# Performance work log

Measured on AMD Instinct MI355X. Metric: run time of the kernel, lower is better.

The kernel has to match this reference:

```python
import jax, jax.numpy as jnp
import numpy as np

LEVEL_SHAPES = [(100, 134), (50, 67), (25, 34), (13, 17)]  # (H, W) per feature level
NH, NL, NP, D, DFF = 8, 4, 4, 256, 1024
DH = D // NH
LTOT = sum(h * w for h, w in LEVEL_SHAPES)  # 17821
BS, NQ = 4, 300


def _ln(x, w, b):
    m = x.mean(-1, keepdims=True)
    v = ((x - m) ** 2).mean(-1, keepdims=True)
    return (x - m) / jnp.sqrt(v + 1e-5) * w + b


def _mha(q, k, v, in_w, in_b, out_w, out_b):
    B, N, _ = q.shape
    wq, wk, wv = jnp.split(in_w, 3, axis=0)
    bq, bk, bv = jnp.split(in_b, 3)
    qh = (q @ wq.T + bq).reshape(B, N, NH, DH)
    kh = (k @ wk.T + bk).reshape(B, N, NH, DH)
    vh = (v @ wv.T + bv).reshape(B, N, NH, DH)
    a = jax.nn.softmax(jnp.einsum('bqhd,bkhd->bhqk', qh, kh) / float(np.sqrt(DH)), axis=-1)
    o = jnp.einsum('bhqk,bkhd->bqhd', a, vh).reshape(B, N, D)
    return o @ out_w.T + out_b


def _bilinear(img, grid):
    # img [B,C,H,W]; grid [B,N,2] in [-1,1]; align_corners=False, zero padding
    B, C, H, W = img.shape
    x = (grid[..., 0] + 1.0) * 0.5 * W - 0.5
    y = (grid[..., 1] + 1.0) * 0.5 * H - 0.5
    x0f = jnp.floor(x); y0f = jnp.floor(y)
    wx = x - x0f; wy = y - y0f
    x0 = x0f.astype(jnp.int32); y0 = y0f.astype(jnp.int32)
    flat = img.reshape(B, C, H * W)

    def gather(xi, yi):
        m = ((xi >= 0) & (xi < W) & (yi >= 0) & (yi < H)).astype(img.dtype)
        idx = jnp.clip(yi, 0, H - 1) * W + jnp.clip(xi, 0, W - 1)
        g = jnp.take_along_axis(flat, jnp.broadcast_to(idx[:, None, :], (B, C, idx.shape[-1])), axis=2)
        return g * m[:, None, :]

    return (gather(x0, y0) * ((1 - wx) * (1 - wy))[:, None]
            + gather(x0 + 1, y0) * (wx * (1 - wy))[:, None]
            + gather(x0, y0 + 1) * ((1 - wx) * wy)[:, None]
            + gather(x0 + 1, y0 + 1) * (wx * wy)[:, None])


def _msdeform(value, loc, aw):
    # value [B,L,NH,DH]; loc [B,Nq,NH,NL,NP,2] in [0,1]; aw [B,Nq,NH,NL,NP]
    B, Nq = loc.shape[0], loc.shape[1]
    outs = []
    start = 0
    for l, (Hl, Wl) in enumerate(LEVEL_SHAPES):
        v = value[:, start:start + Hl * Wl].transpose(0, 2, 3, 1).reshape(B * NH, DH, Hl, Wl)
        g = (2.0 * loc[:, :, :, l] - 1.0).transpose(0, 2, 1, 3, 4).reshape(B * NH, Nq * NP, 2)
        outs.append(_bilinear(v, g).reshape(B * NH, DH, Nq, NP))
        start += Hl * Wl
    samp = jnp.stack(outs, axis=3)  # [B*NH, DH, Nq, NL, NP]
    w = aw.transpose(0, 2, 1, 3, 4).reshape(B * NH, 1, Nq, NL, NP)
    out = (samp * w).sum(axis=(3, 4))  # [B*NH, DH, Nq]
    return out.reshape(B, NH, DH, Nq).transpose(0, 3, 1, 2).reshape(B, Nq, D)


def _deform_branch(q, ref, src_other, vw, vb, ow, ob, aww, awb, outw, outb):
    B, Nq, _ = q.shape
    value = (src_other @ vw.T + vb).reshape(B, -1, NH, DH)
    off = (q @ ow.T + ob).reshape(B, Nq, NH, NL, NP, 2)
    aw = jax.nn.softmax((q @ aww.T + awb).reshape(B, Nq, NH, NL * NP), axis=-1).reshape(B, Nq, NH, NL, NP)
    norm = jnp.array([[w, h] for h, w in LEVEL_SHAPES], dtype=q.dtype)  # (W,H) per level
    loc = ref[:, :, None, :, None, :] + off / norm[None, None, None, :, None, :]
    return _msdeform(value, loc, aw) @ outw.T + outb


def reference(tgt_RGB, tgt_T, query_pos_RGB, query_pos_T, ref_RGB, ref_T, src_RGB, src_T,
              sa_in_w, sa_in_b, sa_out_w, sa_out_b, ln_w, ln_b,
              ffn_w1, ffn_b1, ffn_w2, ffn_b2,
              val_w, val_b, off_w, off_b, aw_w, aw_b, cout_w, cout_b):
    # --- dual self-attention (eval mode: dropout = identity) ---
    q_RGB = tgt_RGB + query_pos_RGB
    q_T = tgt_T + query_pos_T
    sa_RGB = _mha(q_RGB, q_RGB, tgt_RGB, sa_in_w[0], sa_in_b[0], sa_out_w[0], sa_out_b[0])
    sa_T = _mha(q_T, q_T, tgt_T, sa_in_w[1], sa_in_b[1], sa_out_w[1], sa_out_b[1])
    tgt_RGB = _ln(tgt_RGB + sa_RGB, ln_w[0, 1], ln_b[0, 1])  # norm2_RGB
    tgt_T = _ln(tgt_T + sa_T, ln_w[1, 1], ln_b[1, 1])        # norm2_T
    # --- interactive multi-scale deformable cross-attn: RGB queries sample T memory & vice versa ---
    qc_RGB = tgt_RGB + query_pos_RGB
    qc_T = tgt_T + query_pos_T
    t2_RGB = _deform_branch(qc_RGB, ref_RGB, src_T, val_w[0], val_b[0], off_w[0], off_b[0], aw_w[0], aw_b[0], cout_w[0], cout_b[0])
    t2_T = _deform_branch(qc_T, ref_T, src_RGB, val_w[1], val_b[1], off_w[1], off_b[1], aw_w[1], aw_b[1], cout_w[1], cout_b[1])
    F_RGB, F_T = t2_RGB, t2_T
    # cross residuals exactly as in the torch layer (note the modality swap)
    r = tgt_T + t2_RGB
    t = r + t2_T
    tgt_RGB = _ln(r, ln_w[0, 0], ln_b[0, 0])  # norm1_RGB
    tgt_T = _ln(t, ln_w[1, 0], ln_b[1, 0])    # norm1_T
    # --- FFNs ---
    tgt_RGB = _ln(tgt_RGB + (jax.nn.relu(tgt_RGB @ ffn_w1[0].T + ffn_b1[0]) @ ffn_w2[0].T + ffn_b2[0]), ln_w[0, 2], ln_b[0, 2])
    tgt_T = _ln(tgt_T + (jax.nn.relu(tgt_T @ ffn_w1[1].T + ffn_b1[1]) @ ffn_w2[1].T + ffn_b2[1]), ln_w[1, 2], ln_b[1, 2])
    return tgt_RGB, tgt_T, F_RGB, F_T


def setup_inputs() -> dict:
    key = jax.random.key(0)
    ks = jax.random.split(key, 24)
    s = 0.05
    w = lambda k, shp: jax.random.normal(k, shp, dtype=jnp.float32) * s
    return {
        'tgt_RGB': jax.random.normal(ks[0], (BS, NQ, D), jnp.float32),
        'tgt_T': jax.random.normal(ks[1], (BS, NQ, D), jnp.float32),
        'query_pos_RGB': jax.random.normal(ks[2], (BS, NQ, D), jnp.float32),
        'query_pos_T': jax.random.normal(ks[3], (BS, NQ, D), jnp.float32),
        'ref_RGB': jax.random.uniform(ks[4], (BS, NQ, NL, 2), jnp.float32),
        'ref_T': jax.random.uniform(ks[5], (BS, NQ, NL, 2), jnp.float32),
        'src_RGB': jax.random.normal(ks[6], (BS, LTOT, D), jnp.float32),
        'src_T': jax.random.normal(ks[7], (BS, LTOT, D), jnp.float32),
        'sa_in_w': w(ks[8], (2, 3 * D, D)),
        'sa_in_b': jnp.zeros((2, 3 * D), jnp.float32),
        'sa_out_w': w(ks[9], (2, D, D)),
        'sa_out_b': jnp.zeros((2, D), jnp.float32),
        'ln_w': jnp.ones((2, 3, D), jnp.float32),
        'ln_b': jnp.zeros((2, 3, D), jnp.float32),
        'ffn_w1': w(ks[10], (2, DFF, D)),
        'ffn_b1': jnp.zeros((2, DFF), jnp.float32),
        'ffn_w2': w(ks[11], (2, D, DFF)),
        'ffn_b2': jnp.zeros((2, D), jnp.float32),
        'val_w': w(ks[12], (2, D, D)),
        'val_b': jnp.zeros((2, D), jnp.float32),
        'off_w': w(ks[13], (2, NH * NL * NP * 2, D)),
        'off_b': jax.random.normal(ks[14], (2, NH * NL * NP * 2), jnp.float32) * 0.5,
        'aw_w': w(ks[15], (2, NH * NL * NP, D)),
        'aw_b': jnp.zeros((2, NH * NL * NP), jnp.float32),
        'cout_w': w(ks[16], (2, D, D)),
        'cout_b': jnp.zeros((2, D), jnp.float32),
    }
```

## Files before the change

kernel.cpp:

```cpp
#include <hip/hip_runtime.h>
#include <hip/hip_bf16.h>
#include <cstddef>
#include <math.h>

#define NTOK 1200
#define LTOT_C 17821
#define MVAL 71284
#define STOK (NTOK * 256)

typedef __attribute__((ext_vector_type(8))) short bhalf8;
typedef __attribute__((ext_vector_type(4))) float f32x4;

static __device__ __forceinline__ short f2bf(float f) {
    unsigned u = __builtin_bit_cast(unsigned, f);
    u += 0x7fffu + ((u >> 16) & 1u);
    return (short)(u >> 16);
}
static __device__ __forceinline__ float bf2f(short s) {
    unsigned u = ((unsigned)(unsigned short)s) << 16;
    return __builtin_bit_cast(float, u);
}
static __device__ __forceinline__ bhalf8 cvt8(float4 a, float4 b) {
    bhalf8 h;
    h[0] = f2bf(a.x); h[1] = f2bf(a.y); h[2] = f2bf(a.z); h[3] = f2bf(a.w);
    h[4] = f2bf(b.x); h[5] = f2bf(b.y); h[6] = f2bf(b.z); h[7] = f2bf(b.w);
    return h;
}
static __device__ __forceinline__ void gload_lds16(const void* g, void* l) {
    __builtin_amdgcn_global_load_lds(
        (const __attribute__((address_space(1))) void*)g,
        (__attribute__((address_space(3))) void*)l, 16, 0, 0);
}

struct PrepArgs {
    const float* s[10]; short* d[10]; int n[10];
    const float* tgt0; const float* tgt1; const float* pos0; const float* pos1;
    short* qb_bf; short* tgtb;
    const float* off_b; const float* aw_b; float* baw;
};
__global__ __launch_bounds__(256) void prep_all(PrepArgs a) {
    const int task = blockIdx.y;
    if (task < 10) {
        const float* s = a.s[task];
        short* d = a.d[task];
        const int n = a.n[task];
        for (int base = (blockIdx.x * 256 + threadIdx.x) * 8; base < n;
             base += gridDim.x * 256 * 8) {
            const float4 f0 = *reinterpret_cast<const float4*>(s + base);
            const float4 f1 = *reinterpret_cast<const float4*>(s + base + 4);
            *reinterpret_cast<bhalf8*>(d + base) = cvt8(f0, f1);
        }
        return;
    }
    const int z = task - 10;
    if (blockIdx.x == 0 && z == 0) {
        for (int i = threadIdx.x; i < 768; i += 256) {
            const int zz = i / 384, j = i - zz * 384;
            a.baw[i] = (j < 256) ? a.off_b[zz * 256 + j] : a.aw_b[zz * 128 + (j - 256)];
        }
    }
    const float* tg = z ? a.tgt1 : a.tgt0;
    const float* ps = z ? a.pos1 : a.pos0;
    const int base = (blockIdx.x * 256 + threadIdx.x) * 8;
    if (base >= STOK) return;
    const float4 t0 = *reinterpret_cast<const float4*>(tg + base);
    const float4 t1 = *reinterpret_cast<const float4*>(tg + base + 4);
    const float4 p0 = *reinterpret_cast<const float4*>(ps + base);
    const float4 p1 = *reinterpret_cast<const float4*>(ps + base + 4);
    float4 s0 = make_float4(t0.x + p0.x, t0.y + p0.y, t0.z + p0.z, t0.w + p0.w);
    float4 s1 = make_float4(t1.x + p1.x, t1.y + p1.y, t1.z + p1.z, t1.w + p1.w);
    *reinterpret_cast<bhalf8*>(a.qb_bf + (size_t)z * STOK + base) = cvt8(s0, s1);
    *reinterpret_cast<bhalf8*>(a.tgtb + (size_t)z * STOK + base) = cvt8(t0, t1);
}

__global__ __launch_bounds__(256) void val_inproj(
    const float* __restrict__ A0, const float* __restrict__ A1,
    const short* __restrict__ val_bf, const float* __restrict__ val_b,
    short* __restrict__ valb,
    const short* __restrict__ qb_bf, const short* __restrict__ tgtb,
    const short* __restrict__ sa_in_bf, const float* __restrict__ sa_in_b,
    float* __restrict__ qkv)
{
    __shared__ alignas(16) short As[64 * 64];
    __shared__ alignas(16) short Bs[2][128 * 64];
    const int t = threadIdx.x;
    const int wave = t >> 6, lane = t & 63;
    const int l15 = lane & 15, l4 = lane >> 4;
    const int wr = wave >> 1, wc = wave & 1;
    const int nr8 = lane >> 3, q8 = lane & 7;
    const int bi = blockIdx.x;

    if (bi >= 228) {
        const int i = bi - 228;
        const int widx = (i & 7) * 557 + (i >> 3);
        const int x = widx & 1;
        const int yz = widx >> 1;
        const int z = yz / 1114;
        const int y = yz - z * 1114;
        const float* A = z ? A1 : A0;
        const short* W = val_bf + (size_t)z * 65536;
        const float* bz = val_b + z * 256;
        short* Cz = valb + (size_t)z * MVAL * 256;
        const int bm = y * 64, bn = x * 128;
        f32x4 acc[2][4] = {};

        auto stageW = [&](int k0, int buf) {
            #pragma unroll
            for (int ii = 0; ii < 4; ++ii) {
                const int c = wave * 4 + ii;
                const int n = c * 8 + nr8;
                gload_lds16(W + (size_t)(bn + n) * 256 + k0 + ((q8 ^ nr8) << 3),
                            (char*)&Bs[buf][0] + c * 1024);
            }
        };
        float4 paf[2][2];
        auto issueA = [&](int k0) {
            #pragma unroll
            for (int ii = 0; ii < 2; ++ii) {
                const int G = t + ii * 256;
                const int m = G >> 3, g = G & 7;
                const int row = min(bm + m, MVAL - 1);
                const float* s = A + (size_t)row * 256 + k0 + g * 8;
                paf[ii][0] = *reinterpret_cast<const float4*>(s);
                paf[ii][1] = *reinterpret_cast<const float4*>(s + 4);
            }
        };
        auto commitA = [&]() {
            #pragma unroll
            for (int ii = 0; ii < 2; ++ii) {
                const int G = t + ii * 256;
                const int m = G >> 3, g = G & 7;
                *reinterpret_cast<bhalf8*>(&As[m * 64 + ((g ^ (m & 7)) << 3)]) =
                    cvt8(paf[ii][0], paf[ii][1]);
            }
        };
        auto compute = [&](int wbuf) {
            #pragma unroll
            for (int kf = 0; kf < 2; ++kf) {
                bhalf8 af[2], bfv[4];
                #pragma unroll
                for (int mf = 0; mf < 2; ++mf) {
                    const int m = wr * 32 + (mf << 4) + l15;
                    const int g = ((kf << 2) + l4) ^ (m & 7);
                    af[mf] = *reinterpret_cast<const bhalf8*>(&As[m * 64 + (g << 3)]);
                }
                #pragma unroll
                for (int nf = 0; nf < 4; ++nf) {
                    const int n = (wc << 6) + (nf << 4) + l15;
                    const int g = ((kf << 2) + l4) ^ (n & 7);
                    bfv[nf] = *reinterpret_cast<const bhalf8*>(&Bs[wbuf][n * 64 + (g << 3)]);
                }
                #pragma unroll
                for (int mf = 0; mf < 2; ++mf)
                    #pragma unroll
                    for (int nf = 0; nf < 4; ++nf)
                        acc[mf][nf] = __builtin_amdgcn_mfma_f32_16x16x32_bf16(
                            af[mf], bfv[nf], acc[mf][nf], 0, 0, 0);
            }
        };

        issueA(0);
        stageW(0, 0);
        commitA();
        __syncthreads();
        #pragma unroll
        for (int ks = 0; ks < 4; ++ks) {
            const int cur = ks & 1, nxt = cur ^ 1;
            if (ks + 1 < 4) {
                issueA((ks + 1) << 6);
                stageW((ks + 1) << 6, nxt);
            }
            compute(cur);
            if (ks + 1 < 4) {
                __syncthreads();
                commitA();
                __syncthreads();
            }
        }

        float br[4];
        #pragma unroll
        for (int nf = 0; nf < 4; ++nf) br[nf] = bz[bn + (wc << 6) + (nf << 4) + l15];
        #pragma unroll
        for (int mf = 0; mf < 2; ++mf) {
            #pragma unroll
            for (int j = 0; j < 4; ++j) {
                const int row = bm + wr * 32 + (mf << 4) + (l4 << 2) + j;
                if (row >= MVAL) continue;
                const int colbase = bn + (wc << 6);
                #pragma unroll
                for (int nf = 0; nf < 4; ++nf)
                    Cz[(size_t)row * 256 + colbase + (nf << 4) + l15] =
                        f2bf(acc[mf][nf][j] + br[nf]);
            }
        }
    } else {
        const int z = bi / 114;
        const int r = bi - z * 114;
        const int x = r / 19;
        const int y = r - x * 19;
        const short* Abase = ((x < 4) ? qb_bf : tgtb) + (size_t)z * STOK;
        const short* W = sa_in_bf + (size_t)z * 196608;
        const float* bz = sa_in_b + z * 768;
        const int bm = y * 64, bn = x * 128;
        f32x4 acc[2][4] = {};

        auto stageW = [&](int k0, int buf) {
            #pragma unroll
            for (int ii = 0; ii < 4; ++ii) {
                const int c = wave * 4 + ii;
                const int n = c * 8 + nr8;
                gload_lds16(W + (size_t)(bn + n) * 256 + k0 + ((q8 ^ nr8) << 3),
                            (char*)&Bs[buf][0] + c * 1024);
            }
        };
        bhalf8 pab[2];
        auto issueA = [&](int k0) {
            #pragma unroll
            for (int ii = 0; ii < 2; ++ii) {
                const int G = t + ii * 256;
                const int m = G >> 3, g = G & 7;
                const int row = min(bm + m, NTOK - 1);
                pab[ii] = *reinterpret_cast<const bhalf8*>(
                    Abase + (size_t)row * 256 + k0 + g * 8);
            }
        };
        auto commitA = [&]() {
            #pragma unroll
            for (int ii = 0; ii < 2; ++ii) {
                const int G = t + ii * 256;
                const int m = G >> 3, g = G & 7;
                *reinterpret_cast<bhalf8*>(&As[m * 64 + ((g ^ (m & 7)) << 3)]) = pab[ii];
            }
        };
        auto compute = [&](int wbuf) {
            #pragma unroll
            for (int kf = 0; kf < 2; ++kf) {
                bhalf8 af[2], bfv[4];
                #pragma unroll
                for (int mf = 0; mf < 2; ++mf) {
                    const int m = wr * 32 + (mf << 4) + l15;
                    const int g = ((kf << 2) + l4) ^ (m & 7);
                    af[mf] = *reinterpret_cast<const bhalf8*>(&As[m * 64 + (g << 3)]);
                }
                #pragma unroll
                for (int nf = 0; nf < 4; ++nf) {
                    const int n = (wc << 6) + (nf << 4) + l15;
                    const int g = ((kf << 2) + l4) ^ (n & 7);
                    bfv[nf] = *reinterpret_cast<const bhalf8*>(&Bs[wbuf][n * 64 + (g << 3)]);
                }
                #pragma unroll
                for (int mf = 0; mf < 2; ++mf)
                    #pragma unroll
                    for (int nf = 0; nf < 4; ++nf)
                        acc[mf][nf] = __builtin_amdgcn_mfma_f32_16x16x32_bf16(
                            af[mf], bfv[nf], acc[mf][nf], 0, 0, 0);
            }
        };

        issueA(0);
        stageW(0, 0);
        commitA();
        __syncthreads();
        #pragma unroll
        for (int ks = 0; ks < 4; ++ks) {
            const int cur = ks & 1, nxt = cur ^ 1;
            if (ks + 1 < 4) {
                issueA((ks + 1) << 6);
                stageW((ks + 1) << 6, nxt);
            }
            compute(cur);
            if (ks + 1 < 4) {
                __syncthreads();
                commitA();
                __syncthreads();
            }
        }

        float* Cz = qkv + (size_t)z * 921600;
        float br[4];
        #pragma unroll
        for (int nf = 0; nf < 4; ++nf) br[nf] = bz[bn + (wc << 6) + (nf << 4) + l15];
        #pragma unroll
        for (int mf = 0; mf < 2; ++mf) {
            #pragma unroll
            for (int j = 0; j < 4; ++j) {
                const int row = bm + wr * 32 + (mf << 4) + (l4 << 2) + j;
                if (row >= NTOK) continue;
                const int colbase = bn + (wc << 6);
                #pragma unroll
                for (int nf = 0; nf < 4; ++nf)
                    Cz[(size_t)row * 768 + colbase + (nf << 4) + l15] = acc[mf][nf][j] + br[nf];
            }
        }
    }
}

template<bool HASRES, bool RELU, bool OUT_BF16, int BM, int NK>
__global__ __launch_bounds__(256) void gemm_bf16(
    const short* __restrict__ Av, size_t aStrideZ, int lda,
    const short* __restrict__ Wv, size_t wStrideZ, int ldw,
    const float* __restrict__ bias, size_t biasStrideZ,
    const float* __restrict__ Res0, const float* __restrict__ Res1, int ldr,
    void* __restrict__ Cv, size_t cStrideZ, int ldc,
    int M)
{
    constexpr int MFR = BM / 32;
    constexpr int ACW = BM / 32;
    __shared__ alignas(16) short As[2][BM * 64];
    __shared__ alignas(16) short Bs[2][128 * 64];
    const int z = blockIdx.z;
    const short* W = Wv + (size_t)z * wStrideZ;
    const float* bz = bias + (size_t)z * biasStrideZ;
    const int t = threadIdx.x;
    const int wave = t >> 6, lane = t & 63;
    const int l15 = lane & 15, l4 = lane >> 4;
    const int wr = wave >> 1, wc = wave & 1;
    const int bm = blockIdx.y * BM, bn = blockIdx.x * 128;
    f32x4 acc[MFR][4] = {};

    const int nr8 = lane >> 3, q8 = lane & 7;
    auto stageW = [&](int k0, int buf) {
        #pragma unroll
        for (int i = 0; i < 4; ++i) {
            const int c = wave * 4 + i;
            const int n = c * 8 + nr8;
            gload_lds16(W + (size_t)(bn + n) * ldw + k0 + ((q8 ^ nr8) << 3),
                        (char*)&Bs[buf][0] + c * 1024);
        }
    };
    auto stageA = [&](int k0, int buf) {
        #pragma unroll
        for (int i = 0; i < ACW; ++i) {
            const int c = wave * ACW + i;
            const int m = c * 8 + nr8;
            const int row = min(bm + m, M - 1);
            gload_lds16(Av + (size_t)z * aStrideZ + (size_t)row * lda + k0 + ((q8 ^ (m & 7)) << 3),
                        (char*)&As[buf][0] + c * 1024);
        }
    };
    auto compute = [&](int buf) {
        #pragma unroll
        for (int kf = 0; kf < 2; ++kf) {
            bhalf8 af[MFR], bfv[4];
            #pragma unroll
            for (int mf = 0; mf < MFR; ++mf) {
                const int m = wr * (BM / 2) + (mf << 4) + l15;
                const int g = ((kf << 2) + l4) ^ (m & 7);
                af[mf] = *reinterpret_cast<const bhalf8*>(&As[buf][m * 64 + (g << 3)]);
            }
            #pragma unroll
            for (int nf = 0; nf < 4; ++nf) {
                const int n = (wc << 6) + (nf << 4) + l15;
                const int g = ((kf << 2) + l4) ^ (n & 7);
                bfv[nf] = *reinterpret_cast<const bhalf8*>(&Bs[buf][n * 64 + (g << 3)]);
            }
            #pragma unroll
            for (int mf = 0; mf < MFR; ++mf)
                #pragma unroll
                for (int nf = 0; nf < 4; ++nf)
                    acc[mf][nf] = __builtin_amdgcn_mfma_f32_16x16x32_bf16(
                        af[mf], bfv[nf], acc[mf][nf], 0, 0, 0);
        }
    };

    stageA(0, 0);
    stageW(0, 0);
    __syncthreads();
    #pragma unroll
    for (int ks = 0; ks < NK; ++ks) {
        const int cur = ks & 1, nxt = cur ^ 1;
        if (ks + 1 < NK) {
            stageA((ks + 1) << 6, nxt);
            stageW((ks + 1) << 6, nxt);
        }
        compute(cur);
        __syncthreads();
    }

    const float* Rz = HASRES ? (z ? Res1 : Res0) : nullptr;
    float br[4];
    #pragma unroll
    for (int nf = 0; nf < 4; ++nf) br[nf] = bz[bn + (wc << 6) + (nf << 4) + l15];
    #pragma unroll
    for (int mf = 0; mf < MFR; ++mf) {
        #pragma unroll
        for (int j = 0; j < 4; ++j) {
            const int row = bm + wr * (BM / 2) + (mf << 4) + (l4 << 2) + j;
            if (row >= M) continue;
            const int colbase = bn + (wc << 6);
            #pragma unroll
            for (int nf = 0; nf < 4; ++nf) {
                const int col = colbase + (nf << 4) + l15;
                float v = acc[mf][nf][j] + br[nf];
                if (HASRES) v += Rz[(size_t)row * ldr + col];
                if (RELU) v = fmaxf(v, 0.f);
                if (OUT_BF16)
                    ((short*)Cv + (size_t)z * cStrideZ)[(size_t)row * ldc + col] = f2bf(v);
                else
                    ((float*)Cv + (size_t)z * cStrideZ)[(size_t)row * ldc + col] = v;
            }
        }
    }
}

__global__ __launch_bounds__(256) void attn2_kernel(
    const float* __restrict__ qkv_base, short* __restrict__ out_base)
{
    const float scale = 0.17677669529663687f;
    const float* qkv = qkv_base + (size_t)blockIdx.z * 921600;
    short* outp = out_base + (size_t)blockIdx.z * STOK;
    const int b = blockIdx.y >> 3, h = blockIdx.y & 7;
    const int t = threadIdx.x;
    const int ql = t & 31;
    const int kg = t >> 5;
    const int q = blockIdx.x * 32 + ql;
    const bool act = q < 300;
    const float* base = qkv + (size_t)b * 300 * 768;

    float qreg[32];
    if (act) {
        const float4* qp = reinterpret_cast<const float4*>(base + (size_t)q * 768 + h * 32);
        #pragma unroll
        for (int d4 = 0; d4 < 8; ++d4) {
            const float4 v = qp[d4];
            qreg[d4 * 4 + 0] = v.x; qreg[d4 * 4 + 1] = v.y;
            qreg[d4 * 4 + 2] = v.z; qreg[d4 * 4 + 3] = v.w;
        }
    }
    __shared__ float Ks[64][32];
    __shared__ float Vs[64][32];
    float m = -1e30f, l = 0.f, o[32];
    #pragma unroll
    for (int d = 0; d < 32; ++d) o[d] = 0.f;

    for (int k0 = 0; k0 < 300; k0 += 64) {
        const int cnt = min(64, 300 - k0);
        __syncthreads();
        for (int i = t; i < cnt * 32; i += 256) {
            const int kr = i >> 5, d = i & 31;
            Ks[kr][d] = base[(size_t)(k0 + kr) * 768 + 256 + h * 32 + d];
            Vs[kr][d] = base[(size_t)(k0 + kr) * 768 + 512 + h * 32 + d];
        }
        __syncthreads();
        if (act) {
            for (int kk = kg; kk < cnt; kk += 8) {
                const float4* krow = reinterpret_cast<const float4*>(&Ks[kk][0]);
                float s = 0.f;
                #pragma unroll
                for (int d4 = 0; d4 < 8; ++d4) {
                    const float4 kv = krow[d4];
                    s += qreg[d4 * 4 + 0] * kv.x + qreg[d4 * 4 + 1] * kv.y
                       + qreg[d4 * 4 + 2] * kv.z + qreg[d4 * 4 + 3] * kv.w;
                }
                s *= scale;
                const float4* vrow = reinterpret_cast<const float4*>(&Vs[kk][0]);
                if (s <= m) {
                    const float e = __expf(s - m);
                    l += e;
                    #pragma unroll
                    for (int d4 = 0; d4 < 8; ++d4) {
                        const float4 vv = vrow[d4];
                        o[d4 * 4 + 0] += e * vv.x; o[d4 * 4 + 1] += e * vv.y;
                        o[d4 * 4 + 2] += e * vv.z; o[d4 * 4 + 3] += e * vv.w;
                    }
                } else {
                    const float c = __expf(m - s);
                    l = l * c + 1.f;
                    #pragma unroll
                    for (int d4 = 0; d4 < 8; ++d4) {
                        const float4 vv = vrow[d4];
                        o[d4 * 4 + 0] = o[d4 * 4 + 0] * c + vv.x;
                        o[d4 * 4 + 1] = o[d4 * 4 + 1] * c + vv.y;
                        o[d4 * 4 + 2] = o[d4 * 4 + 2] * c + vv.z;
                        o[d4 * 4 + 3] = o[d4 * 4 + 3] * c + vv.w;
                    }
                    m = s;
                }
            }
        }
    }
    __shared__ float pm[32][8];
    __shared__ float pl[32][8];
    __shared__ float po[8][32][33];
    pm[ql][kg] = m; pl[ql][kg] = l;
    #pragma unroll
    for (int d = 0; d < 32; ++d) po[kg][d][ql] = o[d];
    __syncthreads();
    if (kg == 0) {
        float M = pm[ql][0];
        #pragma unroll
        for (int i = 1; i < 8; ++i) M = fmaxf(M, pm[ql][i]);
        float L = 0.f;
        #pragma unroll
        for (int i = 0; i < 8; ++i) L += pl[ql][i] * __expf(pm[ql][i] - M);
        const float invL = 1.f / L;
        #pragma unroll
        for (int i = 0; i < 8; ++i) pm[ql][i] = __expf(pm[ql][i] - M) * invL;
    }
    __syncthreads();
    if (act) {
        #pragma unroll
        for (int dd = 0; dd < 4; ++dd) {
            const int d = kg * 4 + dd;
            float v = 0.f;
            #pragma unroll
            for (int i = 0; i < 8; ++i) v += pm[ql][i] * po[i][d][ql];
            outp[((size_t)b * 300 + q) * 256 + h * 32 + d] = f2bf(v);
        }
    }
}

#define LN_BODY(vexpr, widx)                                                  \
    const int row = blockIdx.x, t = threadIdx.x, z = blockIdx.y;              \
    (void)z;                                                                  \
    const int i = row * 256 + t;                                              \
    const float v = (vexpr);                                                  \
    __shared__ float r1[4], r2[4];                                            \
    float s = v;                                                              \
    _Pragma("unroll")                                                         \
    for (int o = 32; o; o >>= 1) s += __shfl_xor(s, o);                       \
    if ((t & 63) == 0) r1[t >> 6] = s;                                        \
    __syncthreads();                                                          \
    const float mean = (r1[0] + r1[1] + r1[2] + r1[3]) * (1.f / 256.f);       \
    const float dd = v - mean;                                                \
    float sq = dd * dd;                                                       \
    _Pragma("unroll")                                                         \
    for (int o = 32; o; o >>= 1) sq += __shfl_xor(sq, o);                     \
    if ((t & 63) == 0) r2[t >> 6] = sq;                                       \
    __syncthreads();                                                          \
    const float var = (r2[0] + r2[1] + r2[2] + r2[3]) * (1.f / 256.f);        \
    const float y = dd * rsqrtf(var + 1e-5f) * ln_w[(widx) * 256 + t]         \
                    + ln_b[(widx) * 256 + t];

__global__ __launch_bounds__(256) void ln2_fused(
    const float* __restrict__ presum, const float* __restrict__ pos0,
    const float* __restrict__ pos1, const float* __restrict__ ln_w,
    const float* __restrict__ ln_b, short* __restrict__ qc_bf,
    float* __restrict__ tgt2T)
{
    LN_BODY(presum[(size_t)z * STOK + i], z * 3 + 1)
    const float* pos = z ? pos1 : pos0;
    qc_bf[(size_t)z * STOK + i] = f2bf(y + pos[i]);
    if (z == 1) tgt2T[i] = y;
}

__global__ __launch_bounds__(256) void ln1_fused(
    const float* __restrict__ tgt2T, const float* __restrict__ out2,
    const float* __restrict__ out3, const float* __restrict__ ln_w,
    const float* __restrict__ ln_b, short* __restrict__ ln1b,
    float* __restrict__ ln1f)
{
    LN_BODY(tgt2T[row * 256 + t] + out2[row * 256 + t] + (z ? out3[row * 256 + t] : 0.f), z * 3 + 0)
    ln1b[(size_t)z * STOK + i] = f2bf(y);
    ln1f[(size_t)z * STOK + i] = y;
}

__global__ __launch_bounds__(256) void ln3_kernel(
    const float* __restrict__ ffny, const float* __restrict__ ln_w,
    const float* __restrict__ ln_b, float* __restrict__ o0,
    float* __restrict__ o1)
{
    LN_BODY(ffny[(size_t)z * STOK + i], z * 3 + 2)
    (z ? o1 : o0)[i] = y;
}

__global__ __launch_bounds__(256) void sample_kernel(
    const short* __restrict__ valb, const float* __restrict__ oaw,
    const float* __restrict__ ref0, const float* __restrict__ ref1,
    short* __restrict__ out)
{
    const int HL[4] = {100, 50, 25, 13};
    const int WL[4] = {134, 67, 34, 17};
    const int ST[4] = {0, 13400, 16750, 17600};
    const int z = blockIdx.y;
    const int t = threadIdx.x;
    const int wave = t >> 6, lane = t & 63;
    const int qi = wave >> 1, hh = wave & 1;
    const int pg = lane >> 4;
    const int h4 = (lane >> 2) & 3;
    const int dl2 = lane & 3;
    const int h = hh * 4 + h4;
    const int bq = blockIdx.x * 2 + qi;
    const int b = bq / 300;
    const float* op = oaw + ((size_t)z * NTOK + bq) * 384;
    const float* offp = op + h * 32;
    const float* awp  = op + 256 + h * 16;
    const float* refp = (z ? ref1 : ref0) + (size_t)bq * 8;
    const short* vb = valb + (size_t)z * MVAL * 256 + (size_t)b * LTOT_C * 256;
    const int co = h * 32 + dl2 * 8;

    float w16[16];
    float mx = -1e30f;
    #pragma unroll
    for (int i = 0; i < 16; ++i) { w16[i] = awp[i]; mx = fmaxf(mx, w16[i]); }
    float ssum = 0.f;
    #pragma unroll
    for (int i = 0; i < 16; ++i) { w16[i] = __expf(w16[i] - mx); ssum += w16[i]; }
    const float sinv = 1.f / ssum;

    float a[8] = {};
    auto tap = [&](bool cond, int ridx, float wv) {
        if (cond) {
            const bhalf8 sv = *reinterpret_cast<const bhalf8*>(vb + (size_t)ridx * 256 + co);
            #pragma unroll
            for (int dd = 0; dd < 8; ++dd) a[dd] += wv * bf2f(sv[dd]);
        }
    };
    #pragma unroll
    for (int l = 0; l < 4; ++l) {
        const int Wl = WL[l], Hl = HL[l];
        const float rx = refp[l * 2] * (float)Wl - 0.5f;
        const float ry = refp[l * 2 + 1] * (float)Hl - 0.5f;
        const float px = rx + offp[(l * 4 + pg) * 2];
        const float py = ry + offp[(l * 4 + pg) * 2 + 1];
        const float wgt = w16[l * 4 + pg] * sinv;
        const float x0f = floorf(px), y0f = floorf(py);
        const float wx = px - x0f, wy = py - y0f;
        const int x0 = (int)x0f, y0 = (int)y0f;
        const bool xa = (x0 >= 0) & (x0 < Wl);
        const bool xb = (x0 >= -1) & (x0 < Wl - 1);
        const bool ya = (y0 >= 0) & (y0 < Hl);
        const bool yb = (y0 >= -1) & (y0 < Hl - 1);
        const int rbase = ST[l] + y0 * Wl + x0;
        tap(ya & xa, rbase,          wgt * (1.f - wx) * (1.f - wy));
        tap(ya & xb, rbase + 1,      wgt * wx * (1.f - wy));
        tap(yb & xa, rbase + Wl,     wgt * (1.f - wx) * wy);
        tap(yb & xb, rbase + Wl + 1, wgt * wx * wy);
    }
    #pragma unroll
    for (int dd = 0; dd < 8; ++dd) {
        a[dd] += __shfl_xor(a[dd], 16);
        a[dd] += __shfl_xor(a[dd], 32);
    }
    if (pg == 0) {
        bhalf8 o8;
        #pragma unroll
        for (int dd = 0; dd < 8; ++dd) o8[dd] = f2bf(a[dd]);
        *reinterpret_cast<bhalf8*>(&out[((size_t)z * NTOK + bq) * 256 + co]) = o8;
    }
}

extern "C" void kernel_launch(void* const* d_in, const int* in_sizes, int n_in,
                              void* d_out, int out_size, void* d_ws, size_t ws_size,
                              hipStream_t stream) {
    const float* tgt[2] = {(const float*)d_in[0], (const float*)d_in[1]};
    const float* pos[2] = {(const float*)d_in[2], (const float*)d_in[3]};
    const float* ref[2] = {(const float*)d_in[4], (const float*)d_in[5]};
    const float* src[2] = {(const float*)d_in[6], (const float*)d_in[7]};
    const float* sa_in_w  = (const float*)d_in[8];
    const float* sa_in_b  = (const float*)d_in[9];
    const float* sa_out_w = (const float*)d_in[10];
    const float* sa_out_b = (const float*)d_in[11];
    const float* ln_w = (const float*)d_in[12];
    const float* ln_b = (const float*)d_in[13];
    const float* ffn_w1 = (const float*)d_in[14];
    const float* ffn_b1 = (const float*)d_in[15];
    const float* ffn_w2 = (const float*)d_in[16];
    const float* ffn_b2 = (const float*)d_in[17];
    const float* val_w = (const float*)d_in[18];
    const float* val_b = (const float*)d_in[19];
    const float* off_w = (const float*)d_in[20];
    const float* off_b = (const float*)d_in[21];
    const float* aw_w = (const float*)d_in[22];
    const float* aw_b = (const float*)d_in[23];
    const float* cout_w = (const float*)d_in[24];
    const float* cout_b = (const float*)d_in[25];

    char* base = (char*)d_ws;
    size_t off = 0;
    auto alloc = [&](size_t bytes) -> char* {
        char* p = base + off;
        off += (bytes + 255) & ~(size_t)255;
        return p;
    };
    short* wbf   = (short*)alloc((size_t)2031616 * 2);
    float* baw   = (float*)alloc(768 * 4);
    short* qb_bf = (short*)alloc((size_t)2 * STOK * 2);
    short* tgtb  = (short*)alloc((size_t)2 * STOK * 2);
    float* qkv   = (float*)alloc((size_t)2 * 921600 * 4);
    short* attno = (short*)alloc((size_t)2 * STOK * 2);
    float* presum= (float*)alloc((size_t)2 * STOK * 4);
    short* qc_bf = (short*)alloc((size_t)2 * STOK * 2);
    float* tgt2T = (float*)alloc((size_t)STOK * 4);
    float* oawb  = (float*)alloc((size_t)2 * NTOK * 384 * 4);
    short* valb  = (short*)alloc((size_t)2 * MVAL * 256 * 2);
    short* samp  = (short*)alloc((size_t)2 * STOK * 2);
    short* ln1b  = (short*)alloc((size_t)2 * STOK * 2);
    float* ln1f  = (float*)alloc((size_t)2 * STOK * 4);
    short* ffnh  = (short*)alloc((size_t)2 * NTOK * 1024 * 2);
    float* ffny  = (float*)alloc((size_t)2 * STOK * 4);

    short* sa_in_bf  = wbf + 0;
    short* sa_out_bf = wbf + 393216;
    short* ffn1_bf   = wbf + 524288;
    short* ffn2_bf   = wbf + 1048576;
    short* val_bf    = wbf + 1572864;
    short* cout_bf   = wbf + 1703936;
    short* oaw_bf    = wbf + 1835008;

    float* out0 = (float*)d_out;
    float* out1 = out0 + STOK;
    float* out2 = out1 + STOK;
    float* out3 = out2 + STOK;

    const dim3 b256(256);

    PrepArgs pa;
    pa.s[0] = sa_in_w;        pa.d[0] = sa_in_bf;       pa.n[0] = 393216;
    pa.s[1] = sa_out_w;       pa.d[1] = sa_out_bf;      pa.n[1] = 131072;
    pa.s[2] = ffn_w1;         pa.d[2] = ffn1_bf;        pa.n[2] = 524288;
    pa.s[3] = ffn_w2;         pa.d[3] = ffn2_bf;        pa.n[3] = 524288;
    pa.s[4] = val_w;          pa.d[4] = val_bf;         pa.n[4] = 131072;
    pa.s[5] = cout_w;         pa.d[5] = cout_bf;        pa.n[5] = 131072;
    pa.s[6] = off_w;          pa.d[6] = oaw_bf;         pa.n[6] = 65536;
    pa.s[7] = aw_w;           pa.d[7] = oaw_bf + 65536; pa.n[7] = 32768;
    pa.s[8] = off_w + 65536;  pa.d[8] = oaw_bf + 98304; pa.n[8] = 65536;
    pa.s[9] = aw_w + 32768;   pa.d[9] = oaw_bf + 163840;pa.n[9] = 32768;
    pa.tgt0 = tgt[0]; pa.tgt1 = tgt[1]; pa.pos0 = pos[0]; pa.pos1 = pos[1];
    pa.qb_bf = qb_bf; pa.tgtb = tgtb;
    pa.off_b = off_b; pa.aw_b = aw_b; pa.baw = baw;
    prep_all<<<dim3(150, 12), b256, 0, stream>>>(pa);

    val_inproj<<<dim3(4684), b256, 0, stream>>>(
        src[1], src[0], val_bf, val_b, valb,
        qb_bf, tgtb, sa_in_bf, sa_in_b, qkv);

    attn2_kernel<<<dim3(10, 32, 2), b256, 0, stream>>>(qkv, attno);

    gemm_bf16<true, false, false, 64, 4><<<dim3(2, 19, 2), b256, 0, stream>>>(
        attno, (size_t)STOK, 256, sa_out_bf, 65536, 256, sa_out_b, 256,
        tgt[0], tgt[1], 256, presum, (size_t)STOK, 256, NTOK);

    ln2_fused<<<dim3(NTOK, 2), b256, 0, stream>>>(presum, pos[0], pos[1], ln_w, ln_b, qc_bf, tgt2T);

    gemm_bf16<false, false, false, 64, 4><<<dim3(3, 19, 2), b256, 0, stream>>>(
        qc_bf, (size_t)STOK, 256, oaw_bf, 98304, 256, baw, 384,
        nullptr, nullptr, 0, oawb, (size_t)NTOK * 384, 384, NTOK);

    sample_kernel<<<dim3(600, 2), b256, 0, stream>>>(valb, oawb, ref[0], ref[1], samp);

    gemm_bf16<false, false, false, 64, 4><<<dim3(2, 19, 2), b256, 0, stream>>>(
        samp, (size_t)STOK, 256, cout_bf, 65536, 256, cout_b, 256,
        nullptr, nullptr, 0, out2, (size_t)STOK, 256, NTOK);

    ln1_fused<<<dim3(NTOK, 2), b256, 0, stream>>>(tgt2T, out2, out3, ln_w, ln_b, ln1b, ln1f);

    gemm_bf16<false, true, true, 64, 4><<<dim3(8, 19, 2), b256, 0, stream>>>(
        ln1b, (size_t)STOK, 256, ffn1_bf, 262144, 256, ffn_b1, 1024,
        nullptr, nullptr, 0, ffnh, (size_t)NTOK * 1024, 1024, NTOK);

    gemm_bf16<true, false, false, 64, 16><<<dim3(2, 19, 2), b256, 0, stream>>>(
        ffnh, (size_t)NTOK * 1024, 1024, ffn2_bf, 262144, 1024, ffn_b2, 256,
        ln1f, ln1f + STOK, 256, ffny, (size_t)STOK, 256, NTOK);

    ln3_kernel<<<dim3(NTOK, 2), b256, 0, stream>>>(ffny, ln_w, ln_b, out0, out1);
}
```

Measured before the change: 178.4 us.

## Fuse LayerNorm into full-row GEMM epilogues for out-proj and FFN2

Adds a gemm_ln kernel in which each block computes all 256 output columns for 64 rows, so the residual add and LayerNorm can be done in the epilogue with a cross-wave shared-memory reduction. It replaces the sa_out GEMM plus ln2_fused and the FFN2 GEMM plus ln3_kernel. This removes two launches and the fp32 intermediate round trips. In exchange the grid shrinks to 38 blocks (from 76), the W tile is loaded with no double buffering, and variance is computed as E[x^2]-mean^2.

```diff
diff --git a/kernel.cpp b/kernel.cpp
--- a/kernel.cpp
+++ b/kernel.cpp
@@ -399,6 +399,160 @@
                     ((short*)Cv + (size_t)z * cStrideZ)[(size_t)row * ldc + col] = f2bf(v);
                 else
                     ((float*)Cv + (size_t)z * cStrideZ)[(size_t)row * ldc + col] = v;
+            }
+        }
+    }
+}
+
+template<int NK, int MODE>
+__global__ __launch_bounds__(256) void gemm_ln(
+    const short* __restrict__ Av, size_t aStrideZ, int lda,
+    const short* __restrict__ Wv, size_t wStrideZ,
+    const float* __restrict__ bias,
+    const float* __restrict__ Res0, const float* __restrict__ Res1,
+    const float* __restrict__ ln_w, const float* __restrict__ ln_b,
+    const float* __restrict__ pos0, const float* __restrict__ pos1,
+    short* __restrict__ qc_bf, float* __restrict__ tgt2T,
+    float* __restrict__ out0, float* __restrict__ out1,
+    int M)
+{
+    __shared__ alignas(16) short As[64 * 64];
+    __shared__ alignas(16) short Bs[256 * 64];
+    __shared__ float red[2][4][64];
+    const int z = blockIdx.z;
+    const short* W = Wv + (size_t)z * wStrideZ;
+    const float* bz = bias + (size_t)z * 256;
+    const float* Rz = z ? Res1 : Res0;
+    const int li = z * 3 + (MODE == 0 ? 1 : 2);
+    const int t = threadIdx.x;
+    const int wave = t >> 6, lane = t & 63;
+    const int l15 = lane & 15, l4 = lane >> 4;
+    const int nr8 = lane >> 3, q8 = lane & 7;
+    const int bm = blockIdx.y * 64;
+    f32x4 acc[4][4] = {};
+
+    auto stageW = [&](int k0) {
+        #pragma unroll
+        for (int i = 0; i < 8; ++i) {
+            const int c = wave * 8 + i;
+            const int n = c * 8 + nr8;
+            gload_lds16(W + (size_t)n * lda + k0 + ((q8 ^ nr8) << 3),
+                        (char*)&Bs[0] + c * 1024);
+        }
+    };
+    bhalf8 pab[2];
+    auto issueA = [&](int k0) {
+        #pragma unroll
+        for (int ii = 0; ii < 2; ++ii) {
+            const int G = t + ii * 256;
+            const int m = G >> 3, g = G & 7;
+            const int row = min(bm + m, M - 1);
+            pab[ii] = *reinterpret_cast<const bhalf8*>(
+                Av + (size_t)z * aStrideZ + (size_t)row * lda + k0 + g * 8);
+        }
+    };
+    auto commitA = [&]() {
+        #pragma unroll
+        for (int ii = 0; ii < 2; ++ii) {
+            const int G = t + ii * 256;
+            const int m = G >> 3, g = G & 7;
+            *reinterpret_cast<bhalf8*>(&As[m * 64 + ((g ^ (m & 7)) << 3)]) = pab[ii];
+        }
+    };
+    auto compute = [&]() {
+        #pragma unroll
+        for (int kf = 0; kf < 2; ++kf) {
+            bhalf8 af[4], bfv[4];
+            #pragma unroll
+            for (int mf = 0; mf < 4; ++mf) {
+                const int m = (mf << 4) + l15;
+                const int g = ((kf << 2) + l4) ^ (m & 7);
+                af[mf] = *reinterpret_cast<const bhalf8*>(&As[m * 64 + (g << 3)]);
+            }
+            #pragma unroll
+            for (int nf = 0; nf < 4; ++nf) {
+                const int n = (wave << 6) + (nf << 4) + l15;
+                const int g = ((kf << 2) + l4) ^ (n & 7);
+                bfv[nf] = *reinterpret_cast<const bhalf8*>(&Bs[n * 64 + (g << 3)]);
+            }
+            #pragma unroll
+            for (int mf = 0; mf < 4; ++mf)
+                #pragma unroll
+                for (int nf = 0; nf < 4; ++nf)
+                    acc[mf][nf] = __builtin_amdgcn_mfma_f32_16x16x32_bf16(
+                        af[mf], bfv[nf], acc[mf][nf], 0, 0, 0);
+        }
+    };
+
+    for (int ks = 0; ks < NK; ++ks) {
+        issueA(ks << 6);
+        stageW(ks << 6);
+        commitA();
+        __syncthreads();
+        compute();
+        __syncthreads();
+    }
+
+    float br[4];
+    #pragma unroll
+    for (int nf = 0; nf < 4; ++nf) br[nf] = bz[(wave << 6) + (nf << 4) + l15];
+    #pragma unroll
+    for (int mf = 0; mf < 4; ++mf) {
+        #pragma unroll
+        for (int j = 0; j < 4; ++j) {
+            const int row = bm + (mf << 4) + (l4 << 2) + j;
+            const int rr = min(row, M - 1);
+            #pragma unroll
+            for (int nf = 0; nf < 4; ++nf) {
+                const int col = (wave << 6) + (nf << 4) + l15;
+                acc[mf][nf][j] += br[nf] + Rz[(size_t)rr * 256 + col];
+            }
+        }
+    }
+    #pragma unroll
+    for (int mf = 0; mf < 4; ++mf) {
+        #pragma unroll
+        for (int j = 0; j < 4; ++j) {
+            float s = 0.f, q = 0.f;
+            #pragma unroll
+            for (int nf = 0; nf < 4; ++nf) {
+                const float v = acc[mf][nf][j];
+                s += v; q += v * v;
+            }
+            #pragma unroll
+            for (int o = 1; o < 16; o <<= 1) {
+                s += __shfl_xor(s, o);
+                q += __shfl_xor(q, o);
+            }
+            if (l15 == 0) {
+                const int rl = (mf << 4) + (l4 << 2) + j;
+                red[0][wave][rl] = s;
+                red[1][wave][rl] = q;
+            }
+        }
+    }
+    __syncthreads();
+    const float* posz = (MODE == 0) ? (z ? pos1 : pos0) : nullptr;
+    #pragma unroll
+    for (int mf = 0; mf < 4; ++mf) {
+        #pragma unroll
+        for (int j = 0; j < 4; ++j) {
+            const int rl = (mf << 4) + (l4 << 2) + j;
+            const int row = bm + rl;
+            if (row >= M) continue;
+            const float mean = (red[0][0][rl] + red[0][1][rl] + red[0][2][rl] + red[0][3][rl]) * (1.f / 256.f);
+            const float ex2  = (red[1][0][rl] + red[1][1][rl] + red[1][2][rl] + red[1][3][rl]) * (1.f / 256.f);
+            const float rstd = rsqrtf(ex2 - mean * mean + 1e-5f);
+            #pragma unroll
+            for (int nf = 0; nf < 4; ++nf) {
+                const int col = (wave << 6) + (nf << 4) + l15;
+                const float yv = (acc[mf][nf][j] - mean) * rstd * ln_w[li * 256 + col] + ln_b[li * 256 + col];
+                if (MODE == 0) {
+                    qc_bf[(size_t)z * STOK + (size_t)row * 256 + col] = f2bf(yv + posz[(size_t)row * 256 + col]);
+                    if (z == 1) tgt2T[(size_t)row * 256 + col] = yv;
+                } else {
+                    (z ? out1 : out0)[(size_t)row * 256 + col] = yv;
+                }
             }
         }
     }
@@ -533,18 +687,6 @@
     const float y = dd * rsqrtf(var + 1e-5f) * ln_w[(widx) * 256 + t]         \
                     + ln_b[(widx) * 256 + t];
 
-__global__ __launch_bounds__(256) void ln2_fused(
-    const float* __restrict__ presum, const float* __restrict__ pos0,
-    const float* __restrict__ pos1, const float* __restrict__ ln_w,
-    const float* __restrict__ ln_b, short* __restrict__ qc_bf,
-    float* __restrict__ tgt2T)
-{
-    LN_BODY(presum[(size_t)z * STOK + i], z * 3 + 1)
-    const float* pos = z ? pos1 : pos0;
-    qc_bf[(size_t)z * STOK + i] = f2bf(y + pos[i]);
-    if (z == 1) tgt2T[i] = y;
-}
-
 __global__ __launch_bounds__(256) void ln1_fused(
     const float* __restrict__ tgt2T, const float* __restrict__ out2,
     const float* __restrict__ out3, const float* __restrict__ ln_w,
@@ -554,15 +696,6 @@
     LN_BODY(tgt2T[row * 256 + t] + out2[row * 256 + t] + (z ? out3[row * 256 + t] : 0.f), z * 3 + 0)
     ln1b[(size_t)z * STOK + i] = f2bf(y);
     ln1f[(size_t)z * STOK + i] = y;
-}
-
-__global__ __launch_bounds__(256) void ln3_kernel(
-    const float* __restrict__ ffny, const float* __restrict__ ln_w,
-    const float* __restrict__ ln_b, float* __restrict__ o0,
-    float* __restrict__ o1)
-{
-    LN_BODY(ffny[(size_t)z * STOK + i], z * 3 + 2)
-    (z ? o1 : o0)[i] = y;
 }
 
 __global__ __launch_bounds__(256) void sample_kernel(
@@ -680,7 +813,6 @@
     short* tgtb  = (short*)alloc((size_t)2 * STOK * 2);
     float* qkv   = (float*)alloc((size_t)2 * 921600 * 4);
     short* attno = (short*)alloc((size_t)2 * STOK * 2);
-    float* presum= (float*)alloc((size_t)2 * STOK * 4);
     short* qc_bf = (short*)alloc((size_t)2 * STOK * 2);
     float* tgt2T = (float*)alloc((size_t)STOK * 4);
     float* oawb  = (float*)alloc((size_t)2 * NTOK * 384 * 4);
@@ -689,7 +821,6 @@
     short* ln1b  = (short*)alloc((size_t)2 * STOK * 2);
     float* ln1f  = (float*)alloc((size_t)2 * STOK * 4);
     short* ffnh  = (short*)alloc((size_t)2 * NTOK * 1024 * 2);
-    float* ffny  = (float*)alloc((size_t)2 * STOK * 4);
 
     short* sa_in_bf  = wbf + 0;
     short* sa_out_bf = wbf + 393216;
@@ -728,11 +859,10 @@
 
     attn2_kernel<<<dim3(10, 32, 2), b256, 0, stream>>>(qkv, attno);
 
-    gemm_bf16<true, false, false, 64, 4><<<dim3(2, 19, 2), b256, 0, stream>>>(
-        attno, (size_t)STOK, 256, sa_out_bf, 65536, 256, sa_out_b, 256,
-        tgt[0], tgt[1], 256, presum, (size_t)STOK, 256, NTOK);
-
-    ln2_fused<<<dim3(NTOK, 2), b256, 0, stream>>>(presum, pos[0], pos[1], ln_w, ln_b, qc_bf, tgt2T);
+    gemm_ln<4, 0><<<dim3(1, 19, 2), b256, 0, stream>>>(
+        attno, (size_t)STOK, 256, sa_out_bf, 65536, sa_out_b,
+        tgt[0], tgt[1], ln_w, ln_b, pos[0], pos[1],
+        qc_bf, tgt2T, nullptr, nullptr, NTOK);
 
     gemm_bf16<false, false, false, 64, 4><<<dim3(3, 19, 2), b256, 0, stream>>>(
         qc_bf, (size_t)STOK, 256, oaw_bf, 98304, 256, baw, 384,
@@ -750,9 +880,8 @@
         ln1b, (size_t)STOK, 256, ffn1_bf, 262144, 256, ffn_b1, 1024,
         nullptr, nullptr, 0, ffnh, (size_t)NTOK * 1024, 1024, NTOK);
 
-    gemm_bf16<true, false, false, 64, 16><<<dim3(2, 19, 2), b256, 0, stream>>>(
-        ffnh, (size_t)NTOK * 1024, 1024, ffn2_bf, 262144, 1024, ffn_b2, 256,
-        ln1f, ln1f + STOK, 256, ffny, (size_t)STOK, 256, NTOK);
-
-    ln3_kernel<<<dim3(NTOK, 2), b256, 0, stream>>>(ffny, ln_w, ln_b, out0, out1);
-}
+    gemm_ln<16, 1><<<dim3(1, 19, 2), b256, 0, stream>>>(
+        ffnh, (size_t)NTOK * 1024, 1024, ffn2_bf, 262144, ffn_b2,
+        ln1f, ln1f + STOK, ln_w, ln_b, nullptr, nullptr,
+        nullptr, nullptr, out0, out1, NTOK);
+}
```

After: 194.3 us. +8.9%, slower.
